# Kernel tuning notes

Hardware: AMD Instinct MI355X
Metric: run time of the kernel (lower is better)

The kernel has to match this reference:

```python
import jax, jax.numpy as jnp
import numpy as np

N_NODES = 100000
N_EDGES = 1600000
D_IN = 64
H = 64        # hidden_channels = [64, 64]
D_DENSE = 128
N_CLASSES = 2


def setup_inputs() -> dict:
    key = jax.random.key(0)
    ks = jax.random.split(key, 10)
    glorot = lambda k, fi, fo: jax.random.normal(k, (fi, fo), jnp.float32) / np.sqrt(fi).astype(np.float32)
    return {
        "x": jax.random.normal(ks[0], (N_NODES, D_IN), jnp.float32),
        "edge_index": jax.random.randint(ks[1], (2, N_EDGES), 0, N_NODES),
        "W1": glorot(ks[2], D_IN, H),
        "b1": jnp.zeros((H,), jnp.float32),
        "W2": glorot(ks[3], H, H),
        "b2": jnp.zeros((H,), jnp.float32),
        "Wd": glorot(ks[4], H, D_DENSE),
        "bd": jnp.zeros((D_DENSE,), jnp.float32),
        "Wo": glorot(ks[5], D_DENSE, N_CLASSES),
        "bo": jnp.zeros((N_CLASSES,), jnp.float32),
    }


def _gcn_conv(x, src, dst, W, b):
    """GCNConv: D^-1/2 (A+I) D^-1/2 (x @ W) + b  (PyG defaults)."""
    n = x.shape[0]
    h = x @ W  # [N, out]
    # degree of A+I counted on destination nodes (self-loop adds 1)
    deg = jax.ops.segment_sum(jnp.ones(src.shape[0], h.dtype), dst, num_segments=n) + 1.0
    dis = jax.lax.rsqrt(deg)  # deg^-1/2, [N]
    norm = dis[src] * dis[dst]  # [E]
    agg = jax.ops.segment_sum(h[src] * norm[:, None], dst, num_segments=n)
    agg = agg + h * (dis * dis)[:, None]  # self-loop contribution
    return agg + b


def reference(x, edge_index, W1, b1, W2, b2, Wd, bd, Wo, bo):
    # dropout omitted (eval mode); relu after each conv and after dense1
    src, dst = edge_index[0], edge_index[1]
    h = jax.nn.relu(_gcn_conv(x, src, dst, W1, b1))
    h = jax.nn.relu(_gcn_conv(h, src, dst, W2, b2))
    h = jax.nn.relu(h @ Wd + bd)
    return h @ Wo + bo
```

## Files before the change

kernel.cpp:

```cpp
#include <hip/hip_runtime.h>

#define NN 100000
#define NE 1600000
#define SHIFT 7
#define BKN 128
#define NBKT 782
#define BSTRIDE 3072
#define EPB 8192
#define NBB 196

typedef unsigned short u16;

__device__ __forceinline__ u16 f2bf(float f) {
  unsigned u = __float_as_uint(f);
  return (u16)((u + 0x7FFFu + ((u >> 16) & 1u)) >> 16);
}
__device__ __forceinline__ float bf2f(u16 v) {
  return __uint_as_float(((unsigned)v) << 16);
}

__global__ __launch_bounds__(1024) void k_zero(int* __restrict__ bcur) {
  bcur[threadIdx.x] = 0;
}

__global__ __launch_bounds__(512) void k_bin(const int* __restrict__ src,
                                             const int* __restrict__ dst,
                                             int* __restrict__ bcur,
                                             unsigned* __restrict__ packed) {
  __shared__ int lc[NBKT];
  __shared__ unsigned stg[EPB];
  __shared__ u16 sb[EPB];
  for (int i = threadIdx.x; i < NBKT; i += 512) lc[i] = 0;
  __syncthreads();
  const int base = blockIdx.x * EPB;
  const int end = (base + EPB < NE) ? base + EPB : NE;
  for (int e = base + threadIdx.x; e < end; e += 512) {
    const int d = dst[e];
    const int s = src[e];
    const int i = e - base;
    stg[i] = ((unsigned)(d & (BKN - 1)) << 24) | (unsigned)s;
    sb[i] = (u16)(d >> SHIFT);
    atomicAdd(&lc[d >> SHIFT], 1);
  }
  __syncthreads();
  for (int i = threadIdx.x; i < NBKT; i += 512) {
    int c = lc[i];
    if (c) lc[i] = atomicAdd(&bcur[i], c);
  }
  __syncthreads();
  const int n = end - base;
  for (int i = threadIdx.x; i < n; i += 512) {
    const int b = sb[i];
    const int pos = atomicAdd(&lc[b], 1);
    if (pos < BSTRIDE) packed[b * BSTRIDE + pos] = stg[i];
  }
}

__global__ __launch_bounds__(256) void k_csr(const unsigned* __restrict__ packed,
                                             const int* __restrict__ bcur,
                                             int2* __restrict__ epos,
                                             float* __restrict__ dis,
                                             int* __restrict__ srcs) {
  __shared__ int lc[BKN];
  __shared__ int sc[BKN];
  __shared__ int cur[BKN];
  const int b = blockIdx.x;
  const int tid = threadIdx.x;
  const int nbase = b << SHIFT;
  const int ebase = b * BSTRIDE;
  int ecnt = bcur[b];
  if (ecnt > BSTRIDE) ecnt = BSTRIDE;
  if (tid < BKN) lc[tid] = 0;
  __syncthreads();
  for (int e = tid; e < ecnt; e += 256)
    atomicAdd(&lc[packed[ebase + e] >> 24], 1);
  __syncthreads();
  if (tid < BKN) sc[tid] = lc[tid];
  for (int off = 1; off < BKN; off <<= 1) {
    __syncthreads();
    int u = (tid < BKN && tid >= off) ? sc[tid - off] : 0;
    __syncthreads();
    if (tid < BKN) sc[tid] += u;
  }
  __syncthreads();
  if (tid < BKN) {
    const int excl = sc[tid] - lc[tid];
    cur[tid] = ebase + excl;
    const int node = nbase + tid;
    if (node < NN) {
      epos[node] = make_int2(ebase + excl, ebase + excl + lc[tid]);
      dis[node] = rsqrtf((float)lc[tid] + 1.0f);
    }
  }
  __syncthreads();
  for (int e = tid; e < ecnt; e += 256) {
    const unsigned p = packed[ebase + e];
    const int pos = atomicAdd(&cur[p >> 24], 1);
    srcs[pos] = (int)(p & 0x00FFFFFFu);
  }
}

template <bool IN_BF16>
__global__ __launch_bounds__(256) void k_mm(const void* __restrict__ in_,
                                            const float* __restrict__ W,
                                            const float* __restrict__ dis,
                                            u16* __restrict__ hs) {
  __shared__ float At[64][132];
  __shared__ float Wl[64][68];
  const int tid = threadIdx.x;
  for (int i = tid; i < 1024; i += 256) {
    const int k = i >> 4, c4 = (i & 15) << 2;
    const float4 w = ((const float4*)W)[i];
    Wl[k][c4] = w.x; Wl[k][c4 + 1] = w.y; Wl[k][c4 + 2] = w.z; Wl[k][c4 + 3] = w.w;
  }
  const int rbase = blockIdx.x << 7;
  if (IN_BF16) {
    const u16* in = (const u16*)in_;
    for (int i = tid; i < 1024; i += 256) {
      const int row = i >> 3, k8 = (i & 7) << 3;
      const int grow = rbase + row;
      uint4 a = make_uint4(0, 0, 0, 0);
      if (grow < NN) a = ((const uint4*)in)[grow * 8 + (i & 7)];
      At[k8 + 0][row] = bf2f((u16)(a.x & 0xFFFF));
      At[k8 + 1][row] = bf2f((u16)(a.x >> 16));
      At[k8 + 2][row] = bf2f((u16)(a.y & 0xFFFF));
      At[k8 + 3][row] = bf2f((u16)(a.y >> 16));
      At[k8 + 4][row] = bf2f((u16)(a.z & 0xFFFF));
      At[k8 + 5][row] = bf2f((u16)(a.z >> 16));
      At[k8 + 6][row] = bf2f((u16)(a.w & 0xFFFF));
      At[k8 + 7][row] = bf2f((u16)(a.w >> 16));
    }
  } else {
    const float* in = (const float*)in_;
    for (int i = tid; i < 2048; i += 256) {
      const int row = i >> 4, k4 = (i & 15) << 2;
      const int grow = rbase + row;
      float4 a = make_float4(0.f, 0.f, 0.f, 0.f);
      if (grow < NN) a = ((const float4*)in)[grow * 16 + (i & 15)];
      At[k4][row] = a.x; At[k4 + 1][row] = a.y; At[k4 + 2][row] = a.z; At[k4 + 3][row] = a.w;
    }
  }
  __syncthreads();
  const int r0 = (tid >> 3) << 2;
  const int c0 = (tid & 7) << 3;
  float acc[4][8] = {};
#pragma unroll 8
  for (int k = 0; k < 64; ++k) {
    const float4 av = *(const float4*)&At[k][r0];
    const float4 b0 = *(const float4*)&Wl[k][c0];
    const float4 b1 = *(const float4*)&Wl[k][c0 + 4];
    const float a[4] = {av.x, av.y, av.z, av.w};
    const float bb[8] = {b0.x, b0.y, b0.z, b0.w, b1.x, b1.y, b1.z, b1.w};
#pragma unroll
    for (int i = 0; i < 4; ++i)
#pragma unroll
      for (int j = 0; j < 8; ++j) acc[i][j] = fmaf(a[i], bb[j], acc[i][j]);
  }
#pragma unroll
  for (int i = 0; i < 4; ++i) {
    const int row = rbase + r0 + i;
    if (row < NN) {
      const float d = dis[row];
      uint4 o;
      o.x = (unsigned)f2bf(acc[i][0] * d) | ((unsigned)f2bf(acc[i][1] * d) << 16);
      o.y = (unsigned)f2bf(acc[i][2] * d) | ((unsigned)f2bf(acc[i][3] * d) << 16);
      o.z = (unsigned)f2bf(acc[i][4] * d) | ((unsigned)f2bf(acc[i][5] * d) << 16);
      o.w = (unsigned)f2bf(acc[i][6] * d) | ((unsigned)f2bf(acc[i][7] * d) << 16);
      *(uint4*)(hs + row * 64 + c0) = o;
    }
  }
}

__global__ __launch_bounds__(256) void k_gather(const u16* __restrict__ hs,
                                                const int2* __restrict__ epos,
                                                const int* __restrict__ srcs,
                                                const float* __restrict__ dis,
                                                const float* __restrict__ b,
                                                u16* __restrict__ v_out) {
  const uint2* hsq = (const uint2*)hs;
  uint2* voq = (uint2*)v_out;
  const int lane = threadIdx.x & 63;
  const int c16 = lane & 15;
  const int g = lane >> 4;
  const int gw = (blockIdx.x * 256 + threadIdx.x) >> 6;
  const int nw = gridDim.x * 4;
  const float4 bq = ((const float4*)b)[c16];
  for (int t = gw; t < NN; t += nw) {
    const int2 ep = epos[t];
    int e = ep.x;
    const int e1 = ep.y;
    const uint2 sv = hsq[t * 16 + c16];
    float s0 = 0.f, s1 = 0.f, s2 = 0.f, s3 = 0.f;
    if (g == 0) {
      s0 = bf2f((u16)(sv.x & 0xFFFF)); s1 = bf2f((u16)(sv.x >> 16));
      s2 = bf2f((u16)(sv.y & 0xFFFF)); s3 = bf2f((u16)(sv.y >> 16));
    }
#define ACC(v) { s0 += bf2f((u16)((v).x & 0xFFFF)); s1 += bf2f((u16)((v).x >> 16)); \
                 s2 += bf2f((u16)((v).y & 0xFFFF)); s3 += bf2f((u16)((v).y >> 16)); }
    for (; e + 32 <= e1; e += 32) {
      uint2 vv[8];
#pragma unroll
      for (int j = 0; j < 8; ++j) vv[j] = hsq[srcs[e + 4 * j + g] * 16 + c16];
#pragma unroll
      for (int j = 0; j < 8; ++j) ACC(vv[j]);
    }
    if (e + 16 <= e1) {
      uint2 vv[4];
#pragma unroll
      for (int j = 0; j < 4; ++j) vv[j] = hsq[srcs[e + 4 * j + g] * 16 + c16];
#pragma unroll
      for (int j = 0; j < 4; ++j) ACC(vv[j]);
      e += 16;
    }
    if (e + 8 <= e1) {
      uint2 vv[2];
#pragma unroll
      for (int j = 0; j < 2; ++j) vv[j] = hsq[srcs[e + 4 * j + g] * 16 + c16];
#pragma unroll
      for (int j = 0; j < 2; ++j) ACC(vv[j]);
      e += 8;
    }
    if (e + 4 <= e1) {
      const uint2 v = hsq[srcs[e + g] * 16 + c16];
      ACC(v);
      e += 4;
    }
    const int rem = e1 - e;
    if (rem > 0) {
      const int ai = e + g;
      const uint2 v = hsq[srcs[(ai < e1) ? ai : e1 - 1] * 16 + c16];
      if (g < rem) ACC(v);
    }
#undef ACC
    s0 += __shfl_xor(s0, 16); s0 += __shfl_xor(s0, 32);
    s1 += __shfl_xor(s1, 16); s1 += __shfl_xor(s1, 32);
    s2 += __shfl_xor(s2, 16); s2 += __shfl_xor(s2, 32);
    s3 += __shfl_xor(s3, 16); s3 += __shfl_xor(s3, 32);
    if (g == 0) {
      const float d = dis[t];
      const float r0 = fmaxf(fmaf(d, s0, bq.x), 0.0f);
      const float r1 = fmaxf(fmaf(d, s1, bq.y), 0.0f);
      const float r2 = fmaxf(fmaf(d, s2, bq.z), 0.0f);
      const float r3 = fmaxf(fmaf(d, s3, bq.w), 0.0f);
      uint2 o;
      o.x = (unsigned)f2bf(r0) | ((unsigned)f2bf(r1) << 16);
      o.y = (unsigned)f2bf(r2) | ((unsigned)f2bf(r3) << 16);
      voq[t * 16 + c16] = o;
    }
  }
}

__global__ __launch_bounds__(256) void k_head(const u16* __restrict__ v2,
                                              const float* __restrict__ Wd,
                                              const float* __restrict__ bd,
                                              const float* __restrict__ Wo,
                                              const float* __restrict__ bo,
                                              float* __restrict__ out) {
  __shared__ float At[64][132];
  __shared__ float Bl[64][132];
  __shared__ float Wol[256];
  __shared__ float bdl[128];
  const int tid = threadIdx.x;
  for (int i = tid; i < 2048; i += 256) {
    const int k = i >> 5, c4 = (i & 31) << 2;
    const float4 w = ((const float4*)Wd)[i];
    Bl[k][c4] = w.x; Bl[k][c4 + 1] = w.y; Bl[k][c4 + 2] = w.z; Bl[k][c4 + 3] = w.w;
  }
  if (tid < 256) Wol[tid] = Wo[tid];
  if (tid < 128) bdl[tid] = bd[tid];
  const int rbase = blockIdx.x << 7;
  for (int i = tid; i < 1024; i += 256) {
    const int row = i >> 3, k8 = (i & 7) << 3;
    const int grow = rbase + row;
    uint4 a = make_uint4(0, 0, 0, 0);
    if (grow < NN) a = ((const uint4*)v2)[grow * 8 + (i & 7)];
    At[k8 + 0][row] = bf2f((u16)(a.x & 0xFFFF));
    At[k8 + 1][row] = bf2f((u16)(a.x >> 16));
    At[k8 + 2][row] = bf2f((u16)(a.y & 0xFFFF));
    At[k8 + 3][row] = bf2f((u16)(a.y >> 16));
    At[k8 + 4][row] = bf2f((u16)(a.z & 0xFFFF));
    At[k8 + 5][row] = bf2f((u16)(a.z >> 16));
    At[k8 + 6][row] = bf2f((u16)(a.w & 0xFFFF));
    At[k8 + 7][row] = bf2f((u16)(a.w >> 16));
  }
  __syncthreads();
  const int r0 = (tid >> 4) << 3;
  const int c0 = (tid & 15) << 3;
  float acc[8][8];
#pragma unroll
  for (int i = 0; i < 8; ++i)
#pragma unroll
    for (int j = 0; j < 8; ++j) acc[i][j] = bdl[c0 + j];
#pragma unroll 4
  for (int k = 0; k < 64; ++k) {
    const float4 a0 = *(const float4*)&At[k][r0];
    const float4 a1 = *(const float4*)&At[k][r0 + 4];
    const float4 b0 = *(const float4*)&Bl[k][c0];
    const float4 b1 = *(const float4*)&Bl[k][c0 + 4];
    const float a[8] = {a0.x, a0.y, a0.z, a0.w, a1.x, a1.y, a1.z, a1.w};
    const float bb[8] = {b0.x, b0.y, b0.z, b0.w, b1.x, b1.y, b1.z, b1.w};
#pragma unroll
    for (int i = 0; i < 8; ++i)
#pragma unroll
      for (int j = 0; j < 8; ++j) acc[i][j] = fmaf(a[i], bb[j], acc[i][j]);
  }
  const float bo0 = bo[0], bo1 = bo[1];
#pragma unroll
  for (int i = 0; i < 8; ++i) {
    float o0 = 0.f, o1 = 0.f;
#pragma unroll
    for (int j = 0; j < 8; ++j) {
      const float t = fmaxf(acc[i][j], 0.f);
      o0 = fmaf(t, Wol[(c0 + j) * 2], o0);
      o1 = fmaf(t, Wol[(c0 + j) * 2 + 1], o1);
    }
#pragma unroll
    for (int m = 1; m < 16; m <<= 1) {
      o0 += __shfl_xor(o0, m);
      o1 += __shfl_xor(o1, m);
    }
    const int row = rbase + r0 + i;
    if ((tid & 15) == 0 && row < NN) {
      out[row * 2 + 0] = o0 + bo0;
      out[row * 2 + 1] = o1 + bo1;
    }
  }
}

extern "C" void kernel_launch(void* const* d_in, const int* in_sizes, int n_in,
                              void* d_out, int out_size, void* d_ws, size_t ws_size,
                              hipStream_t stream) {
  const float* x  = (const float*)d_in[0];
  const int*   ei = (const int*)d_in[1];
  const float* W1 = (const float*)d_in[2];
  const float* b1 = (const float*)d_in[3];
  const float* W2 = (const float*)d_in[4];
  const float* b2 = (const float*)d_in[5];
  const float* Wd = (const float*)d_in[6];
  const float* bd = (const float*)d_in[7];
  const float* Wo = (const float*)d_in[8];
  const float* bo = (const float*)d_in[9];
  float* out = (float*)d_out;

  const int* src = ei;
  const int* dst = ei + NE;

  char* ws = (char*)d_ws;
  int*      bcur  = (int*)(ws);
  int2*     epos  = (int2*)(ws + 1024L * 4);
  float*    dis   = (float*)(ws + 205824L * 4);
  int*      srcs  = (int*)(ws + 308224L * 4);
  u16*      hs    = (u16*)(ws + 2710528L * 4);
  unsigned* packed = (unsigned*)hs;
  u16*      vbuf  = (u16*)(ws + 5912832L * 4);

  k_zero<<<1, 1024, 0, stream>>>(bcur);

  k_bin<<<NBB, 512, 0, stream>>>(src, dst, bcur, packed);
  k_csr<<<NBKT, 256, 0, stream>>>(packed, bcur, epos, dis, srcs);

  k_mm<false><<<NBKT, 256, 0, stream>>>(x, W1, dis, hs);
  k_gather<<<4096, 256, 0, stream>>>(hs, epos, srcs, dis, b1, vbuf);
  k_mm<true><<<NBKT, 256, 0, stream>>>(vbuf, W2, dis, hs);
  k_gather<<<4096, 256, 0, stream>>>(hs, epos, srcs, dis, b2, vbuf);
  k_head<<<NBKT, 256, 0, stream>>>(vbuf, Wd, bd, Wo, bo, out);
}
```

Before: 197.5 us.

## Use bf16 MFMA for node transform and head GEMMs, cache bucket in LDS

Replaces the scalar FP32 FMA inner loops in the per-layer transform and the dense head with 16x16x32 bf16 MFMA instructions, keeping A and transposed weights in LDS as bf16. The float input x and the weights are now rounded to bf16 before multiplication, which reduces accuracy. The CSR build kernel also stages each bucket's packed edges in shared memory so the global array is read once instead of twice. The MFMA output layout writes hs with scattered 2-byte stores instead of 16-byte vector stores, which may cost some store efficiency.

After: 163.3 us. 1.21x faster.

```diff
diff --git a/kernel.cpp b/kernel.cpp
--- a/kernel.cpp
+++ b/kernel.cpp
@@ -10,6 +10,8 @@
 #define NBB 196
 
 typedef unsigned short u16;
+typedef __attribute__((ext_vector_type(8))) short bf16x8;
+typedef __attribute__((ext_vector_type(4))) float f32x4;
 
 __device__ __forceinline__ u16 f2bf(float f) {
   unsigned u = __float_as_uint(f);
@@ -61,6 +63,7 @@
                                              int2* __restrict__ epos,
                                              float* __restrict__ dis,
                                              int* __restrict__ srcs) {
+  __shared__ unsigned pk[BSTRIDE];
   __shared__ int lc[BKN];
   __shared__ int sc[BKN];
   __shared__ int cur[BKN];
@@ -72,8 +75,11 @@
   if (ecnt > BSTRIDE) ecnt = BSTRIDE;
   if (tid < BKN) lc[tid] = 0;
   __syncthreads();
-  for (int e = tid; e < ecnt; e += 256)
-    atomicAdd(&lc[packed[ebase + e] >> 24], 1);
+  for (int e = tid; e < ecnt; e += 256) {
+    const unsigned p = packed[ebase + e];
+    pk[e] = p;
+    atomicAdd(&lc[p >> 24], 1);
+  }
   __syncthreads();
   if (tid < BKN) sc[tid] = lc[tid];
   for (int off = 1; off < BKN; off <<= 1) {
@@ -94,7 +100,7 @@
   }
   __syncthreads();
   for (int e = tid; e < ecnt; e += 256) {
-    const unsigned p = packed[ebase + e];
+    const unsigned p = pk[e];
     const int pos = atomicAdd(&cur[p >> 24], 1);
     srcs[pos] = (int)(p & 0x00FFFFFFu);
   }
@@ -105,68 +111,65 @@
                                             const float* __restrict__ W,
                                             const float* __restrict__ dis,
                                             u16* __restrict__ hs) {
-  __shared__ float At[64][132];
-  __shared__ float Wl[64][68];
+  __shared__ __align__(16) u16 At[128][72];
+  __shared__ __align__(16) u16 Wt[64][72];
   const int tid = threadIdx.x;
+  const int rbase = blockIdx.x << 7;
   for (int i = tid; i < 1024; i += 256) {
     const int k = i >> 4, c4 = (i & 15) << 2;
     const float4 w = ((const float4*)W)[i];
-    Wl[k][c4] = w.x; Wl[k][c4 + 1] = w.y; Wl[k][c4 + 2] = w.z; Wl[k][c4 + 3] = w.w;
-  }
-  const int rbase = blockIdx.x << 7;
+    Wt[c4 + 0][k] = f2bf(w.x); Wt[c4 + 1][k] = f2bf(w.y);
+    Wt[c4 + 2][k] = f2bf(w.z); Wt[c4 + 3][k] = f2bf(w.w);
+  }
   if (IN_BF16) {
     const u16* in = (const u16*)in_;
     for (int i = tid; i < 1024; i += 256) {
-      const int row = i >> 3, k8 = (i & 7) << 3;
+      const int row = i >> 3, c8 = (i & 7) << 3;
       const int grow = rbase + row;
       uint4 a = make_uint4(0, 0, 0, 0);
       if (grow < NN) a = ((const uint4*)in)[grow * 8 + (i & 7)];
-      At[k8 + 0][row] = bf2f((u16)(a.x & 0xFFFF));
-      At[k8 + 1][row] = bf2f((u16)(a.x >> 16));
-      At[k8 + 2][row] = bf2f((u16)(a.y & 0xFFFF));
-      At[k8 + 3][row] = bf2f((u16)(a.y >> 16));
-      At[k8 + 4][row] = bf2f((u16)(a.z & 0xFFFF));
-      At[k8 + 5][row] = bf2f((u16)(a.z >> 16));
-      At[k8 + 6][row] = bf2f((u16)(a.w & 0xFFFF));
-      At[k8 + 7][row] = bf2f((u16)(a.w >> 16));
+      *(uint4*)&At[row][c8] = a;
     }
   } else {
     const float* in = (const float*)in_;
     for (int i = tid; i < 2048; i += 256) {
-      const int row = i >> 4, k4 = (i & 15) << 2;
+      const int row = i >> 4, c4 = (i & 15) << 2;
       const int grow = rbase + row;
       float4 a = make_float4(0.f, 0.f, 0.f, 0.f);
       if (grow < NN) a = ((const float4*)in)[grow * 16 + (i & 15)];
-      At[k4][row] = a.x; At[k4 + 1][row] = a.y; At[k4 + 2][row] = a.z; At[k4 + 3][row] = a.w;
-    }
-  }
-  __syncthreads();
-  const int r0 = (tid >> 3) << 2;
-  const int c0 = (tid & 7) << 3;
-  float acc[4][8] = {};
-#pragma unroll 8
-  for (int k = 0; k < 64; ++k) {
-    const float4 av = *(const float4*)&At[k][r0];
-    const float4 b0 = *(const float4*)&Wl[k][c0];
-    const float4 b1 = *(const float4*)&Wl[k][c0 + 4];
-    const float a[4] = {av.x, av.y, av.z, av.w};
-    const float bb[8] = {b0.x, b0.y, b0.z, b0.w, b1.x, b1.y, b1.z, b1.w};
-#pragma unroll
-    for (int i = 0; i < 4; ++i)
-#pragma unroll
-      for (int j = 0; j < 8; ++j) acc[i][j] = fmaf(a[i], bb[j], acc[i][j]);
-  }
-#pragma unroll
-  for (int i = 0; i < 4; ++i) {
-    const int row = rbase + r0 + i;
-    if (row < NN) {
-      const float d = dis[row];
-      uint4 o;
-      o.x = (unsigned)f2bf(acc[i][0] * d) | ((unsigned)f2bf(acc[i][1] * d) << 16);
-      o.y = (unsigned)f2bf(acc[i][2] * d) | ((unsigned)f2bf(acc[i][3] * d) << 16);
-      o.z = (unsigned)f2bf(acc[i][4] * d) | ((unsigned)f2bf(acc[i][5] * d) << 16);
-      o.w = (unsigned)f2bf(acc[i][6] * d) | ((unsigned)f2bf(acc[i][7] * d) << 16);
-      *(uint4*)(hs + row * 64 + c0) = o;
+      At[row][c4 + 0] = f2bf(a.x); At[row][c4 + 1] = f2bf(a.y);
+      At[row][c4 + 2] = f2bf(a.z); At[row][c4 + 3] = f2bf(a.w);
+    }
+  }
+  __syncthreads();
+  const int lane = tid & 63;
+  const int w = tid >> 6;
+  const int lr = lane & 15;
+  const int lk = lane >> 4;
+  f32x4 acc[2][4] = {};
+#pragma unroll
+  for (int kc = 0; kc < 2; ++kc) {
+    const int kb = kc * 32 + lk * 8;
+    const bf16x8 a0 = *(const bf16x8*)&At[w * 32 + lr][kb];
+    const bf16x8 a1 = *(const bf16x8*)&At[w * 32 + 16 + lr][kb];
+#pragma unroll
+    for (int ct = 0; ct < 4; ++ct) {
+      const bf16x8 bf = *(const bf16x8*)&Wt[ct * 16 + lr][kb];
+      acc[0][ct] = __builtin_amdgcn_mfma_f32_16x16x32_bf16(a0, bf, acc[0][ct], 0, 0, 0);
+      acc[1][ct] = __builtin_amdgcn_mfma_f32_16x16x32_bf16(a1, bf, acc[1][ct], 0, 0, 0);
+    }
+  }
+#pragma unroll
+  for (int rt = 0; rt < 2; ++rt) {
+#pragma unroll
+    for (int r = 0; r < 4; ++r) {
+      const int row = rbase + w * 32 + rt * 16 + lk * 4 + r;
+      if (row < NN) {
+        const float d = dis[row];
+#pragma unroll
+        for (int ct = 0; ct < 4; ++ct)
+          hs[row * 64 + ct * 16 + lr] = f2bf(acc[rt][ct][r] * d);
+      }
     }
   }
 }
@@ -256,73 +259,67 @@
                                               const float* __restrict__ Wo,
                                               const float* __restrict__ bo,
                                               float* __restrict__ out) {
-  __shared__ float At[64][132];
-  __shared__ float Bl[64][132];
+  __shared__ __align__(16) u16 At[128][72];
+  __shared__ __align__(16) u16 Bt[128][72];
   __shared__ float Wol[256];
   __shared__ float bdl[128];
   const int tid = threadIdx.x;
+  const int rbase = blockIdx.x << 7;
   for (int i = tid; i < 2048; i += 256) {
     const int k = i >> 5, c4 = (i & 31) << 2;
     const float4 w = ((const float4*)Wd)[i];
-    Bl[k][c4] = w.x; Bl[k][c4 + 1] = w.y; Bl[k][c4 + 2] = w.z; Bl[k][c4 + 3] = w.w;
+    Bt[c4 + 0][k] = f2bf(w.x); Bt[c4 + 1][k] = f2bf(w.y);
+    Bt[c4 + 2][k] = f2bf(w.z); Bt[c4 + 3][k] = f2bf(w.w);
   }
   if (tid < 256) Wol[tid] = Wo[tid];
   if (tid < 128) bdl[tid] = bd[tid];
-  const int rbase = blockIdx.x << 7;
   for (int i = tid; i < 1024; i += 256) {
-    const int row = i >> 3, k8 = (i & 7) << 3;
+    const int row = i >> 3, c8 = (i & 7) << 3;
     const int grow = rbase + row;
     uint4 a = make_uint4(0, 0, 0, 0);
     if (grow < NN) a = ((const uint4*)v2)[grow * 8 + (i & 7)];
-    At[k8 + 0][row] = bf2f((u16)(a.x & 0xFFFF));
-    At[k8 + 1][row] = bf2f((u16)(a.x >> 16));
-    At[k8 + 2][row] = bf2f((u16)(a.y & 0xFFFF));
-    At[k8 + 3][row] = bf2f((u16)(a.y >> 16));
-    At[k8 + 4][row] = bf2f((u16)(a.z & 0xFFFF));
-    At[k8 + 5][row] = bf2f((u16)(a.z >> 16));
-    At[k8 + 6][row] = bf2f((u16)(a.w & 0xFFFF));
-    At[k8 + 7][row] = bf2f((u16)(a.w >> 16));
-  }
-  __syncthreads();
-  const int r0 = (tid >> 4) << 3;
-  const int c0 = (tid & 15) << 3;
-  float acc[8][8];
-#pragma unroll
-  for (int i = 0; i < 8; ++i)
-#pragma unroll
-    for (int j = 0; j < 8; ++j) acc[i][j] = bdl[c0 + j];
-#pragma unroll 4
-  for (int k = 0; k < 64; ++k) {
-    const float4 a0 = *(const float4*)&At[k][r0];
-    const float4 a1 = *(const float4*)&At[k][r0 + 4];
-    const float4 b0 = *(const float4*)&Bl[k][c0];
-    const float4 b1 = *(const float4*)&Bl[k][c0 + 4];
-    const float a[8] = {a0.x, a0.y, a0.z, a0.w, a1.x, a1.y, a1.z, a1.w};
-    const float bb[8] = {b0.x, b0.y, b0.z, b0.w, b1.x, b1.y, b1.z, b1.w};
-#pragma unroll
-    for (int i = 0; i < 8; ++i)
-#pragma unroll
-      for (int j = 0; j < 8; ++j) acc[i][j] = fmaf(a[i], bb[j], acc[i][j]);
+    *(uint4*)&At[row][c8] = a;
+  }
+  __syncthreads();
+  const int lane = tid & 63;
+  const int w = tid >> 6;
+  const int lr = lane & 15;
+  const int lk = lane >> 4;
+  f32x4 acc[2][8] = {};
+#pragma unroll
+  for (int kc = 0; kc < 2; ++kc) {
+    const int kb = kc * 32 + lk * 8;
+    const bf16x8 a0 = *(const bf16x8*)&At[w * 32 + lr][kb];
+    const bf16x8 a1 = *(const bf16x8*)&At[w * 32 + 16 + lr][kb];
+#pragma unroll
+    for (int ct = 0; ct < 8; ++ct) {
+      const bf16x8 bf = *(const bf16x8*)&Bt[ct * 16 + lr][kb];
+      acc[0][ct] = __builtin_amdgcn_mfma_f32_16x16x32_bf16(a0, bf, acc[0][ct], 0, 0, 0);
+      acc[1][ct] = __builtin_amdgcn_mfma_f32_16x16x32_bf16(a1, bf, acc[1][ct], 0, 0, 0);
+    }
   }
   const float bo0 = bo[0], bo1 = bo[1];
 #pragma unroll
-  for (int i = 0; i < 8; ++i) {
-    float o0 = 0.f, o1 = 0.f;
-#pragma unroll
-    for (int j = 0; j < 8; ++j) {
-      const float t = fmaxf(acc[i][j], 0.f);
-      o0 = fmaf(t, Wol[(c0 + j) * 2], o0);
-      o1 = fmaf(t, Wol[(c0 + j) * 2 + 1], o1);
-    }
-#pragma unroll
-    for (int m = 1; m < 16; m <<= 1) {
-      o0 += __shfl_xor(o0, m);
-      o1 += __shfl_xor(o1, m);
-    }
-    const int row = rbase + r0 + i;
-    if ((tid & 15) == 0 && row < NN) {
-      out[row * 2 + 0] = o0 + bo0;
-      out[row * 2 + 1] = o1 + bo1;
+  for (int rt = 0; rt < 2; ++rt) {
+#pragma unroll
+    for (int r = 0; r < 4; ++r) {
+      const int row = rbase + w * 32 + rt * 16 + lk * 4 + r;
+      float o0 = 0.f, o1 = 0.f;
+#pragma unroll
+      for (int ct = 0; ct < 8; ++ct) {
+        const int j = ct * 16 + lr;
+        const float t = fmaxf(acc[rt][ct][r] + bdl[j], 0.f);
+        o0 = fmaf(t, Wol[j * 2], o0);
+        o1 = fmaf(t, Wol[j * 2 + 1], o1);
+      }
+      o0 += __shfl_xor(o0, 1); o1 += __shfl_xor(o1, 1);
+      o0 += __shfl_xor(o0, 2); o1 += __shfl_xor(o1, 2);
+      o0 += __shfl_xor(o0, 4); o1 += __shfl_xor(o1, 4);
+      o0 += __shfl_xor(o0, 8); o1 += __shfl_xor(o1, 8);
+      if (lr == 0 && row < NN) {
+        out[row * 2 + 0] = o0 + bo0;
+        out[row * 2 + 1] = o1 + bo1;
+      }
     }
   }
 }
```
